# Performance work log

Hardware: AMD Instinct MI355X
Metric: run time of the kernel (lower is better)

The kernel has to match this reference:

```python
import jax, jax.numpy as jnp
import numpy as np

N_NODES = 100000
N_EDGES = 3200000
IN_CH = 128
HID_CH = 128
OUT_CH = 64
N_GRAPHS = 128


def gcn_conv(x, edge_index, edge_weight, W, b):
    # x: [N, F_in]; edge_index: [2, E] (row=source j, col=target i); edge_weight: [E]
    N = x.shape[0]
    x = x @ W  # [N, F_out]
    # add self-loops with weight 1 (PyG GCNConv default, fill_value=1.0)
    loop = jnp.arange(N, dtype=edge_index.dtype)
    row = jnp.concatenate([edge_index[0], loop])
    col = jnp.concatenate([edge_index[1], loop])
    w = jnp.concatenate([edge_weight, jnp.ones((N,), dtype=x.dtype)])
    # symmetric normalization: deg computed at target (col)
    deg = jax.ops.segment_sum(w, col, num_segments=N)
    dinv = jnp.where(deg > 0, jax.lax.rsqrt(deg), 0.0)
    norm = dinv[row] * w * dinv[col]  # [E+N]
    msg = x[row] * norm[:, None]  # gather + scale
    out = jax.ops.segment_sum(msg, col, num_segments=N)  # scatter-add
    return out + b


def setup_inputs() -> dict:
    key = jax.random.key(0)
    ks = jax.random.split(key, 10)
    x = jax.random.normal(ks[0], (N_NODES, IN_CH), dtype=jnp.float32)
    edge_index = jax.random.randint(ks[1], (2, N_EDGES), 0, N_NODES, dtype=jnp.int64)
    edge_attr = jax.random.uniform(ks[2], (N_EDGES,), dtype=jnp.float32)
    batch = jnp.sort(jax.random.randint(ks[3], (N_NODES,), 0, N_GRAPHS, dtype=jnp.int64))
    # GCNConv weights (glorot) and zero bias, classifier xavier_normal + bias 0.1
    def glorot(k, fi, fo):
        s = jnp.sqrt(6.0 / (fi + fo))
        return jax.random.uniform(k, (fi, fo), minval=-s, maxval=s, dtype=jnp.float32)
    W1 = glorot(ks[4], IN_CH, HID_CH)
    b1 = jnp.zeros((HID_CH,), dtype=jnp.float32)
    W2 = glorot(ks[5], HID_CH, HID_CH)
    b2 = jnp.zeros((HID_CH,), dtype=jnp.float32)
    std = jnp.sqrt(2.0 / (HID_CH + OUT_CH))
    Wc = jax.random.normal(ks[6], (HID_CH, OUT_CH), dtype=jnp.float32) * std
    bc = jnp.full((OUT_CH,), 0.1, dtype=jnp.float32)
    return {"x": x, "edge_index": edge_index, "edge_attr": edge_attr,
            "batch": batch, "W1": W1, "b1": b1, "W2": W2, "b2": b2,
            "Wc": Wc, "bc": bc}


def reference(x, edge_index, edge_attr, batch, W1, b1, W2, b2, Wc, bc):
    h = jax.nn.relu(gcn_conv(x, edge_index, edge_attr, W1, b1))
    h = jax.nn.relu(gcn_conv(h, edge_index, edge_attr, W2, b2))
    pooled = jax.ops.segment_sum(h, batch, num_segments=N_GRAPHS)  # [G, HID]
    logits = pooled @ Wc + bc
    return jax.nn.sigmoid(logits)
```

## Files before the change

### kernel.cpp

```cpp
#include <hip/hip_runtime.h>
#include <hip/hip_bf16.h>
#include <hip/hip_fp16.h>


#define FEAT 128
#define OUTC 64
#define PAD  80
#define NB_SHIFT 8
#define BINSZ 256
#define CAP 9216
#define TILE_A 8192
#define CNT_STRIDE 16
#define LDW 136

typedef _Float16 half8 __attribute__((ext_vector_type(8)));
typedef float    f32x4 __attribute__((ext_vector_type(4)));

__global__ __launch_bounds__(256) void bin_edges(const int* __restrict__ ei,
                                                 const float* __restrict__ ew,
                                                 int* __restrict__ binCnt,
                                                 int2* __restrict__ binned,
                                                 int E, int nbins) {
    __shared__ int hist[512];
    __shared__ int base[512];
    int tid = threadIdx.x;
    int e0 = blockIdx.x * TILE_A;
    for (int i = tid; i < nbins; i += 256) hist[i] = 0;
    __syncthreads();
    for (int i = 0; i < TILE_A; i += 256) {
        int e = e0 + i + tid;
        if (e < E) atomicAdd(&hist[ei[E + e] >> NB_SHIFT], 1);
    }
    __syncthreads();
    for (int i = tid; i < nbins; i += 256) {
        int h = hist[i];
        base[i] = (h > 0) ? atomicAdd(&binCnt[i * CNT_STRIDE], h) : 0;
        hist[i] = 0;
    }
    __syncthreads();
    for (int i = 0; i < TILE_A; i += 256) {
        int e = e0 + i + tid;
        if (e < E) {
            int col = ei[E + e];
            int row = ei[e];
            float w = ew[e];
            int b  = col >> NB_SHIFT;
            int lp = atomicAdd(&hist[b], 1);
            int pos = base[b] + lp;
            if (pos < CAP) {
                int cl = col & (BINSZ - 1);
                binned[(size_t)b * CAP + pos] = make_int2((cl << 24) | row, __float_as_int(w));
            }
        }
    }
}

__global__ __launch_bounds__(256) void bin_scatter(const int2* __restrict__ binned,
                                                   const int* __restrict__ binCnt,
                                                   int* __restrict__ cnt,
                                                   int2* __restrict__ buf,
                                                   float* __restrict__ dinv, int N) {
    __shared__ int   lcnt[BINSZ];
    __shared__ float dsum[BINSZ];
    int tid = threadIdx.x;
    int b = blockIdx.x;
    lcnt[tid] = 0;
    dsum[tid] = 0.f;
    __syncthreads();
    int node0 = b << NB_SHIFT;
    int ne = min(binCnt[b * CNT_STRIDE], CAP);
    const int2* src = binned + (size_t)b * CAP;
    for (int i = tid; i < ne; i += 256) {
        int2 m = src[i];
        int cl  = ((unsigned)m.x) >> 24;
        int row = m.x & 0xFFFFFF;
        float wf = __int_as_float(m.y);
        int pos = atomicAdd(&lcnt[cl], 1);
        unsigned short hs = __half_as_ushort(__float2half(wf));
        int wpk = (int)hs | ((int)hs << 16);
        if (pos < PAD) buf[(size_t)(node0 + cl) * PAD + pos] = make_int2(row, wpk);
        unsafeAtomicAdd(&dsum[cl], wf);
    }
    __syncthreads();
    int node = node0 + tid;
    if (node < N) {
        cnt[node]  = min(lcnt[tid], PAD);
        dinv[node] = rsqrtf(1.0f + dsum[tid]);
    }
}

__global__ void wt_prep(const float* __restrict__ W, _Float16* __restrict__ Wt) {
    int i = blockIdx.x * 256 + threadIdx.x;
    int n = i >> 7, k = i & 127;
    Wt[(size_t)n * LDW + k] = (_Float16)W[(size_t)k * FEAT + n];
}

__global__ __launch_bounds__(256) void gemm_mfma(const float* __restrict__ X,
                                                 const _Float16* __restrict__ Wt,
                                                 const float* __restrict__ dinv,
                                                 __half* __restrict__ Y, int N) {
    __shared__ _Float16 sWt[FEAT * LDW];
    int tid  = threadIdx.x;
    int row0 = blockIdx.x * 128;
    {
        const int4* src = (const int4*)Wt;
        int4* dst = (int4*)sWt;
        for (int i = tid; i < (FEAT * LDW) / 8; i += 256) dst[i] = src[i];
    }
    __syncthreads();

    int wave = tid >> 6;
    int lane = tid & 63;
    int m    = lane & 15;
    int quad = lane >> 4;

    f32x4 acc[2][8];
    #pragma unroll
    for (int rt = 0; rt < 2; ++rt)
        #pragma unroll
        for (int ct = 0; ct < 8; ++ct)
            acc[rt][ct] = (f32x4){0.f, 0.f, 0.f, 0.f};

    int rowA[2];
    rowA[0] = min(row0 + wave * 32 + m, N - 1);
    rowA[1] = min(row0 + wave * 32 + 16 + m, N - 1);

    #pragma unroll
    for (int kt = 0; kt < 4; ++kt) {
        int k0 = kt * 32;
        half8 a[2];
        #pragma unroll
        for (int rt = 0; rt < 2; ++rt) {
            const float4* p = (const float4*)(X + (size_t)rowA[rt] * FEAT + k0 + quad * 8);
            float4 f0 = p[0], f1 = p[1];
            half8 h;
            h[0] = (_Float16)f0.x; h[1] = (_Float16)f0.y;
            h[2] = (_Float16)f0.z; h[3] = (_Float16)f0.w;
            h[4] = (_Float16)f1.x; h[5] = (_Float16)f1.y;
            h[6] = (_Float16)f1.z; h[7] = (_Float16)f1.w;
            a[rt] = h;
        }
        #pragma unroll
        for (int ct = 0; ct < 8; ++ct) {
            half8 b = *(const half8*)&sWt[(ct * 16 + m) * LDW + k0 + quad * 8];
            acc[0][ct] = __builtin_amdgcn_mfma_f32_16x16x32_f16(a[0], b, acc[0][ct], 0, 0, 0);
            acc[1][ct] = __builtin_amdgcn_mfma_f32_16x16x32_f16(a[1], b, acc[1][ct], 0, 0, 0);
        }
    }

    #pragma unroll
    for (int rt = 0; rt < 2; ++rt) {
        int lr0 = wave * 32 + rt * 16 + quad * 4;
        #pragma unroll
        for (int r = 0; r < 4; ++r) {
            int gr = row0 + lr0 + r;
            if (gr < N) {
                float d = dinv[gr];
                #pragma unroll
                for (int ct = 0; ct < 8; ++ct)
                    Y[(size_t)gr * FEAT + ct * 16 + m] = __float2half(d * acc[rt][ct][r]);
            }
        }
    }
}

__global__ __launch_bounds__(256) void agg_kernel(const __half* __restrict__ Y,
                                                  const int2* __restrict__ buf,
                                                  const int* __restrict__ cnt,
                                                  const float* __restrict__ dinv,
                                                  const float* __restrict__ bias,
                                                  float* __restrict__ Out, int N) {
    int node = blockIdx.x * 4 + (threadIdx.x >> 6);
    int lane = threadIdx.x & 63;
    if (node >= N) return;
    int grp = lane >> 4;
    int fl  = lane & 15;
    int c = cnt[node];
    const int2* meta = buf + (size_t)node * PAD;

    __half2 z = __floats2half2_rn(0.f, 0.f);
    __half2 a0 = z, a1 = z, a2 = z, a3 = z;
    __half2 b0 = z, b1 = z, b2 = z, b3 = z;

    if (grp == 0) {
        int4 sv = ((const int4*)(Y + (size_t)node * FEAT))[fl];
        a0 = *(const __half2*)&sv.x; a1 = *(const __half2*)&sv.y;
        a2 = *(const __half2*)&sv.z; a3 = *(const __half2*)&sv.w;
    }

    for (int t = 0; t < c; t += 8) {
        int eA = t + grp;
        int eB = t + 4 + grp;
        int2 mA = (eA < c) ? meta[eA] : make_int2(node, 0);
        int2 mB = (eB < c) ? meta[eB] : make_int2(node, 0);
        int4 vA = ((const int4*)(Y + (size_t)mA.x * FEAT))[fl];
        int4 vB = ((const int4*)(Y + (size_t)mB.x * FEAT))[fl];
        __half2 wA = *(const __half2*)&mA.y;
        __half2 wB = *(const __half2*)&mB.y;
        a0 = __hfma2(wA, *(const __half2*)&vA.x, a0);
        a1 = __hfma2(wA, *(const __half2*)&vA.y, a1);
        a2 = __hfma2(wA, *(const __half2*)&vA.z, a2);
        a3 = __hfma2(wA, *(const __half2*)&vA.w, a3);
        b0 = __hfma2(wB, *(const __half2*)&vB.x, b0);
        b1 = __hfma2(wB, *(const __half2*)&vB.y, b1);
        b2 = __hfma2(wB, *(const __half2*)&vB.z, b2);
        b3 = __hfma2(wB, *(const __half2*)&vB.w, b3);
    }

    float2 F0 = __half22float2(a0), F1 = __half22float2(a1);
    float2 F2 = __half22float2(a2), F3 = __half22float2(a3);
    {
        float2 t0 = __half22float2(b0), t1 = __half22float2(b1);
        float2 t2 = __half22float2(b2), t3 = __half22float2(b3);
        F0.x += t0.x; F0.y += t0.y; F1.x += t1.x; F1.y += t1.y;
        F2.x += t2.x; F2.y += t2.y; F3.x += t3.x; F3.y += t3.y;
    }
    float f[8] = {F0.x, F0.y, F1.x, F1.y, F2.x, F2.y, F3.x, F3.y};
    #pragma unroll
    for (int i = 0; i < 8; ++i) {
        f[i] += __shfl_xor(f[i], 16);
        f[i] += __shfl_xor(f[i], 32);
    }
    if (grp == 0) {
        float d = dinv[node];
        int c0 = fl * 8;
        float4 bo0 = *(const float4*)(bias + c0);
        float4 bo1 = *(const float4*)(bias + c0 + 4);
        float4 o0 = {fmaxf(d * f[0] + bo0.x, 0.f), fmaxf(d * f[1] + bo0.y, 0.f),
                     fmaxf(d * f[2] + bo0.z, 0.f), fmaxf(d * f[3] + bo0.w, 0.f)};
        float4 o1 = {fmaxf(d * f[4] + bo1.x, 0.f), fmaxf(d * f[5] + bo1.y, 0.f),
                     fmaxf(d * f[6] + bo1.z, 0.f), fmaxf(d * f[7] + bo1.w, 0.f)};
        *(float4*)(Out + (size_t)node * FEAT + c0)     = o0;
        *(float4*)(Out + (size_t)node * FEAT + c0 + 4) = o1;
    }
}

__global__ void pool_kernel(const float* __restrict__ H, const int* __restrict__ batch,
                            float* __restrict__ pooled, int N, int chunk) {
    int f  = threadIdx.x;
    int n0 = blockIdx.x * chunk;
    if (n0 >= N) return;
    int n1 = min(n0 + chunk, N);
    float acc = 0.f;
    int cur = batch[n0];
    for (int n = n0; n < n1; ++n) {
        int g = batch[n];
        if (g != cur) {
            unsafeAtomicAdd(&pooled[cur * FEAT + f], acc);
            acc = 0.f;
            cur = g;
        }
        acc += H[(size_t)n * FEAT + f];
    }
    unsafeAtomicAdd(&pooled[cur * FEAT + f], acc);
}

__global__ void classify_kernel(const float* __restrict__ pooled, const float* __restrict__ Wc,
                                const float* __restrict__ bc, float* __restrict__ out) {
    int g = blockIdx.x;
    int c = threadIdx.x;
    float acc = bc[c];
    const float* pr = pooled + g * FEAT;
    for (int k = 0; k < FEAT; ++k) acc += pr[k] * Wc[k * OUTC + c];
    out[g * OUTC + c] = 1.0f / (1.0f + expf(-acc));
}

extern "C" void kernel_launch(void* const* d_in, const int* in_sizes, int n_in,
                              void* d_out, int out_size, void* d_ws, size_t ws_size,
                              hipStream_t stream) {
    const float* x     = (const float*)d_in[0];
    const int*   ei    = (const int*)d_in[1];
    const float* ew    = (const float*)d_in[2];
    const int*   batch = (const int*)d_in[3];
    const float* W1    = (const float*)d_in[4];
    const float* b1    = (const float*)d_in[5];
    const float* W2    = (const float*)d_in[6];
    const float* b2    = (const float*)d_in[7];
    const float* Wc    = (const float*)d_in[8];
    const float* bc    = (const float*)d_in[9];
    float* out = (float*)d_out;

    const int N = in_sizes[0] / FEAT;
    const int E = in_sizes[2];
    const int G = out_size / OUTC;
    const int nbins = (N + BINSZ - 1) / BINSZ;

    char* w = (char*)d_ws;
    size_t off = 0;
    auto alloc = [&](size_t bytes) {
        void* p = w + off;
        off = (off + bytes + 255) & ~(size_t)255;
        return p;
    };
    float*     dinv   = (float*)alloc((size_t)N * 4);
    int*       cnt    = (int*)alloc((size_t)N * 4);
    int*       binCnt = (int*)alloc((size_t)nbins * CNT_STRIDE * 4);
    int2*      binned = (int2*)alloc((size_t)nbins * CAP * 8);
    int2*      buf    = (int2*)alloc((size_t)N * PAD * 8);
    __half*    bufY   = (__half*)alloc((size_t)N * FEAT * 2);
    float*     bufH   = (float*)alloc((size_t)N * FEAT * 4);
    float*     pooled = (float*)alloc((size_t)G * FEAT * 4);
    _Float16*  wt1    = (_Float16*)alloc((size_t)FEAT * LDW * 2);
    _Float16*  wt2    = (_Float16*)alloc((size_t)FEAT * LDW * 2);
    (void)ws_size;

    hipMemsetAsync(binCnt, 0, (size_t)nbins * CNT_STRIDE * 4, stream);
    hipMemsetAsync(pooled, 0, (size_t)G * FEAT * 4, stream);

    bin_edges<<<(E + TILE_A - 1) / TILE_A, 256, 0, stream>>>(ei, ew, binCnt, binned, E, nbins);
    bin_scatter<<<nbins, 256, 0, stream>>>(binned, binCnt, cnt, buf, dinv, N);
    wt_prep<<<64, 256, 0, stream>>>(W1, wt1);
    wt_prep<<<64, 256, 0, stream>>>(W2, wt2);

    const int gemm_blocks = (N + 127) / 128;
    const int agg_blocks  = (N + 3) / 4;

    gemm_mfma<<<gemm_blocks, 256, 0, stream>>>(x, wt1, dinv, bufY, N);
    agg_kernel<<<agg_blocks, 256, 0, stream>>>(bufY, buf, cnt, dinv, b1, bufH, N);
    gemm_mfma<<<gemm_blocks, 256, 0, stream>>>(bufH, wt2, dinv, bufY, N);
    agg_kernel<<<agg_blocks, 256, 0, stream>>>(bufY, buf, cnt, dinv, b2, bufH, N);

    const int chunk = 128;
    pool_kernel<<<(N + chunk - 1) / chunk, FEAT, 0, stream>>>(bufH, batch, pooled, N, chunk);
    classify_kernel<<<G, OUTC, 0, stream>>>(pooled, Wc, bc, out);
}
```

Before: 545.7 us.

## Build compact CSR via in-bin sort and store hidden activations in fp16

Replaces the padded per-node edge buffer (80 slots per node) with a compact CSR built by counting-sorting each bin in LDS and writing the result back over the binned array, with per-node offsets. The intermediate hidden activations become fp16 instead of fp32, so the second GEMM reads half8 directly and pooling reads halves. Nontemporal loads and stores are added for edge metadata and outputs. This cuts memory footprint and traffic for the padded buffer and the activations, at the cost of fp16 precision on the hidden layer and a large dynamic LDS allocation per bin block.

```diff
diff --git a/kernel.cpp b/kernel.cpp
--- a/kernel.cpp
+++ b/kernel.cpp
@@ -5,7 +5,6 @@
 
 #define FEAT 128
 #define OUTC 64
-#define PAD  80
 #define NB_SHIFT 8
 #define BINSZ 256
 #define CAP 9216
@@ -15,6 +14,8 @@
 
 typedef _Float16 half8 __attribute__((ext_vector_type(8)));
 typedef float    f32x4 __attribute__((ext_vector_type(4)));
+typedef int      iv2  __attribute__((ext_vector_type(2)));
+typedef int      iv4  __attribute__((ext_vector_type(4)));
 
 __global__ __launch_bounds__(256) void bin_edges(const int* __restrict__ ei,
                                                  const float* __restrict__ ew,
@@ -55,36 +56,53 @@
     }
 }
 
-__global__ __launch_bounds__(256) void bin_scatter(const int2* __restrict__ binned,
-                                                   const int* __restrict__ binCnt,
-                                                   int* __restrict__ cnt,
-                                                   int2* __restrict__ buf,
-                                                   float* __restrict__ dinv, int N) {
-    __shared__ int   lcnt[BINSZ];
+__global__ __launch_bounds__(256) void bin_sort_csr(int2* __restrict__ binned,
+                                                    const int* __restrict__ binCnt,
+                                                    int* __restrict__ offs,
+                                                    int* __restrict__ cnt,
+                                                    float* __restrict__ dinv, int N) {
+    extern __shared__ int2 sE[];
     __shared__ float dsum[BINSZ];
-    int tid = threadIdx.x;
-    int b = blockIdx.x;
-    lcnt[tid] = 0;
+    __shared__ int kh[BINSZ], kb[BINSZ], ksc[BINSZ];
+    int tid = threadIdx.x, b = blockIdx.x;
+    int node0 = b << NB_SHIFT;
     dsum[tid] = 0.f;
-    __syncthreads();
-    int node0 = b << NB_SHIFT;
+    kh[tid] = 0;
+    __syncthreads();
     int ne = min(binCnt[b * CNT_STRIDE], CAP);
-    const int2* src = binned + (size_t)b * CAP;
+    int2* src = binned + (size_t)b * CAP;
     for (int i = tid; i < ne; i += 256) {
         int2 m = src[i];
-        int cl  = ((unsigned)m.x) >> 24;
-        int row = m.x & 0xFFFFFF;
-        float wf = __int_as_float(m.y);
-        int pos = atomicAdd(&lcnt[cl], 1);
-        unsigned short hs = __half_as_ushort(__float2half(wf));
-        int wpk = (int)hs | ((int)hs << 16);
-        if (pos < PAD) buf[(size_t)(node0 + cl) * PAD + pos] = make_int2(row, wpk);
-        unsafeAtomicAdd(&dsum[cl], wf);
-    }
-    __syncthreads();
+        int cl = ((unsigned)m.x) >> 24;
+        atomicAdd(&kh[cl], 1);
+        unsafeAtomicAdd(&dsum[cl], __int_as_float(m.y));
+    }
+    __syncthreads();
+    int v = kh[tid];
+    ksc[tid] = v;
+    __syncthreads();
+    for (int off = 1; off < BINSZ; off <<= 1) {
+        int t = (tid >= off) ? ksc[tid - off] : 0;
+        __syncthreads();
+        ksc[tid] += t;
+        __syncthreads();
+    }
+    kb[tid] = ksc[tid] - v;
+    kh[tid] = 0;
+    __syncthreads();
+    for (int i = tid; i < ne; i += 256) {
+        int2 m = src[i];
+        int cl = ((unsigned)m.x) >> 24;
+        int p = kb[cl] + atomicAdd(&kh[cl], 1);
+        unsigned short hs = __half_as_ushort(__float2half(__int_as_float(m.y)));
+        sE[p] = make_int2(m.x & 0xFFFFFF, (int)hs | ((int)hs << 16));
+    }
+    __syncthreads();
+    for (int i = tid; i < ne; i += 256) src[i] = sE[i];
     int node = node0 + tid;
     if (node < N) {
-        cnt[node]  = min(lcnt[tid], PAD);
+        offs[node] = b * CAP + kb[tid];
+        cnt[node]  = kh[tid];
         dinv[node] = rsqrtf(1.0f + dsum[tid]);
     }
 }
@@ -95,7 +113,8 @@
     Wt[(size_t)n * LDW + k] = (_Float16)W[(size_t)k * FEAT + n];
 }
 
-__global__ __launch_bounds__(256) void gemm_mfma(const float* __restrict__ X,
+template<typename TIn>
+__global__ __launch_bounds__(256) void gemm_mfma(const TIn* __restrict__ X,
                                                  const _Float16* __restrict__ Wt,
                                                  const float* __restrict__ dinv,
                                                  __half* __restrict__ Y, int N) {
@@ -131,14 +150,18 @@
         half8 a[2];
         #pragma unroll
         for (int rt = 0; rt < 2; ++rt) {
-            const float4* p = (const float4*)(X + (size_t)rowA[rt] * FEAT + k0 + quad * 8);
-            float4 f0 = p[0], f1 = p[1];
-            half8 h;
-            h[0] = (_Float16)f0.x; h[1] = (_Float16)f0.y;
-            h[2] = (_Float16)f0.z; h[3] = (_Float16)f0.w;
-            h[4] = (_Float16)f1.x; h[5] = (_Float16)f1.y;
-            h[6] = (_Float16)f1.z; h[7] = (_Float16)f1.w;
-            a[rt] = h;
+            if constexpr (sizeof(TIn) == 4) {
+                const float4* p = (const float4*)((const float*)X + (size_t)rowA[rt] * FEAT + k0 + quad * 8);
+                float4 f0 = p[0], f1 = p[1];
+                half8 h;
+                h[0] = (_Float16)f0.x; h[1] = (_Float16)f0.y;
+                h[2] = (_Float16)f0.z; h[3] = (_Float16)f0.w;
+                h[4] = (_Float16)f1.x; h[5] = (_Float16)f1.y;
+                h[6] = (_Float16)f1.z; h[7] = (_Float16)f1.w;
+                a[rt] = h;
+            } else {
+                a[rt] = *(const half8*)((const _Float16*)X + (size_t)rowA[rt] * FEAT + k0 + quad * 8);
+            }
         }
         #pragma unroll
         for (int ct = 0; ct < 8; ++ct) {
@@ -165,18 +188,19 @@
 }
 
 __global__ __launch_bounds__(256) void agg_kernel(const __half* __restrict__ Y,
-                                                  const int2* __restrict__ buf,
+                                                  const int2* __restrict__ elist,
+                                                  const int* __restrict__ offs,
                                                   const int* __restrict__ cnt,
                                                   const float* __restrict__ dinv,
                                                   const float* __restrict__ bias,
-                                                  float* __restrict__ Out, int N) {
+                                                  __half* __restrict__ Out, int N) {
     int node = blockIdx.x * 4 + (threadIdx.x >> 6);
     int lane = threadIdx.x & 63;
     if (node >= N) return;
     int grp = lane >> 4;
     int fl  = lane & 15;
     int c = cnt[node];
-    const int2* meta = buf + (size_t)node * PAD;
+    const iv2* meta = (const iv2*)(elist + offs[node]);
 
     __half2 z = __floats2half2_rn(0.f, 0.f);
     __half2 a0 = z, a1 = z, a2 = z, a3 = z;
@@ -191,12 +215,13 @@
     for (int t = 0; t < c; t += 8) {
         int eA = t + grp;
         int eB = t + 4 + grp;
-        int2 mA = (eA < c) ? meta[eA] : make_int2(node, 0);
-        int2 mB = (eB < c) ? meta[eB] : make_int2(node, 0);
-        int4 vA = ((const int4*)(Y + (size_t)mA.x * FEAT))[fl];
-        int4 vB = ((const int4*)(Y + (size_t)mB.x * FEAT))[fl];
-        __half2 wA = *(const __half2*)&mA.y;
-        __half2 wB = *(const __half2*)&mB.y;
+        iv2 mA = (eA < c) ? __builtin_nontemporal_load(meta + eA) : (iv2){node, 0};
+        iv2 mB = (eB < c) ? __builtin_nontemporal_load(meta + eB) : (iv2){node, 0};
+        int4 vA = *(const int4*)(Y + (size_t)mA.x * FEAT + fl * 8);
+        int4 vB = *(const int4*)(Y + (size_t)mB.x * FEAT + fl * 8);
+        int wAi = mA.y, wBi = mB.y;
+        __half2 wA = *(const __half2*)&wAi;
+        __half2 wB = *(const __half2*)&wBi;
         a0 = __hfma2(wA, *(const __half2*)&vA.x, a0);
         a1 = __hfma2(wA, *(const __half2*)&vA.y, a1);
         a2 = __hfma2(wA, *(const __half2*)&vA.z, a2);
@@ -226,16 +251,16 @@
         int c0 = fl * 8;
         float4 bo0 = *(const float4*)(bias + c0);
         float4 bo1 = *(const float4*)(bias + c0 + 4);
-        float4 o0 = {fmaxf(d * f[0] + bo0.x, 0.f), fmaxf(d * f[1] + bo0.y, 0.f),
-                     fmaxf(d * f[2] + bo0.z, 0.f), fmaxf(d * f[3] + bo0.w, 0.f)};
-        float4 o1 = {fmaxf(d * f[4] + bo1.x, 0.f), fmaxf(d * f[5] + bo1.y, 0.f),
-                     fmaxf(d * f[6] + bo1.z, 0.f), fmaxf(d * f[7] + bo1.w, 0.f)};
-        *(float4*)(Out + (size_t)node * FEAT + c0)     = o0;
-        *(float4*)(Out + (size_t)node * FEAT + c0 + 4) = o1;
-    }
-}
-
-__global__ void pool_kernel(const float* __restrict__ H, const int* __restrict__ batch,
+        __half2 p01 = __floats2half2_rn(fmaxf(d * f[0] + bo0.x, 0.f), fmaxf(d * f[1] + bo0.y, 0.f));
+        __half2 p23 = __floats2half2_rn(fmaxf(d * f[2] + bo0.z, 0.f), fmaxf(d * f[3] + bo0.w, 0.f));
+        __half2 p45 = __floats2half2_rn(fmaxf(d * f[4] + bo1.x, 0.f), fmaxf(d * f[5] + bo1.y, 0.f));
+        __half2 p67 = __floats2half2_rn(fmaxf(d * f[6] + bo1.z, 0.f), fmaxf(d * f[7] + bo1.w, 0.f));
+        iv4 ov = { *(int*)&p01, *(int*)&p23, *(int*)&p45, *(int*)&p67 };
+        __builtin_nontemporal_store(ov, (iv4*)(Out + (size_t)node * FEAT + c0));
+    }
+}
+
+__global__ void pool_kernel(const __half* __restrict__ H, const int* __restrict__ batch,
                             float* __restrict__ pooled, int N, int chunk) {
     int f  = threadIdx.x;
     int n0 = blockIdx.x * chunk;
@@ -250,7 +275,8 @@
             acc = 0.f;
             cur = g;
         }
-        acc += H[(size_t)n * FEAT + f];
+        unsigned short us = __builtin_nontemporal_load((const unsigned short*)(H + (size_t)n * FEAT + f));
+        acc += __half2float(__ushort_as_half(us));
     }
     unsafeAtomicAdd(&pooled[cur * FEAT + f], acc);
 }
@@ -294,11 +320,11 @@
     };
     float*     dinv   = (float*)alloc((size_t)N * 4);
     int*       cnt    = (int*)alloc((size_t)N * 4);
+    int*       offs   = (int*)alloc((size_t)N * 4);
     int*       binCnt = (int*)alloc((size_t)nbins * CNT_STRIDE * 4);
     int2*      binned = (int2*)alloc((size_t)nbins * CAP * 8);
-    int2*      buf    = (int2*)alloc((size_t)N * PAD * 8);
     __half*    bufY   = (__half*)alloc((size_t)N * FEAT * 2);
-    float*     bufH   = (float*)alloc((size_t)N * FEAT * 4);
+    __half*    bufH   = (__half*)alloc((size_t)N * FEAT * 2);
     float*     pooled = (float*)alloc((size_t)G * FEAT * 4);
     _Float16*  wt1    = (_Float16*)alloc((size_t)FEAT * LDW * 2);
     _Float16*  wt2    = (_Float16*)alloc((size_t)FEAT * LDW * 2);
@@ -308,17 +334,17 @@
     hipMemsetAsync(pooled, 0, (size_t)G * FEAT * 4, stream);
 
     bin_edges<<<(E + TILE_A - 1) / TILE_A, 256, 0, stream>>>(ei, ew, binCnt, binned, E, nbins);
-    bin_scatter<<<nbins, 256, 0, stream>>>(binned, binCnt, cnt, buf, dinv, N);
+    bin_sort_csr<<<nbins, 256, (size_t)CAP * sizeof(int2), stream>>>(binned, binCnt, offs, cnt, dinv, N);
     wt_prep<<<64, 256, 0, stream>>>(W1, wt1);
     wt_prep<<<64, 256, 0, stream>>>(W2, wt2);
 
     const int gemm_blocks = (N + 127) / 128;
     const int agg_blocks  = (N + 3) / 4;
 
-    gemm_mfma<<<gemm_blocks, 256, 0, stream>>>(x, wt1, dinv, bufY, N);
-    agg_kernel<<<agg_blocks, 256, 0, stream>>>(bufY, buf, cnt, dinv, b1, bufH, N);
-    gemm_mfma<<<gemm_blocks, 256, 0, stream>>>(bufH, wt2, dinv, bufY, N);
-    agg_kernel<<<agg_blocks, 256, 0, stream>>>(bufY, buf, cnt, dinv, b2, bufH, N);
+    gemm_mfma<float><<<gemm_blocks, 256, 0, stream>>>(x, wt1, dinv, bufY, N);
+    agg_kernel<<<agg_blocks, 256, 0, stream>>>(bufY, binned, offs, cnt, dinv, b1, bufH, N);
+    gemm_mfma<__half><<<gemm_blocks, 256, 0, stream>>>(bufH, wt2, dinv, bufY, N);
+    agg_kernel<<<agg_blocks, 256, 0, stream>>>(bufY, binned, offs, cnt, dinv, b2, bufH, N);
 
     const int chunk = 128;
     pool_kernel<<<(N + chunk - 1) / chunk, FEAT, 0, stream>>>(bufH, batch, pooled, N, chunk);
```

New measurement: 564.7 us. 3.5% more time.
